# Kernel optimization log

Hardware: AMD Instinct MI355X
Metric: run time of the kernel (lower is better)

## Reference

```python
import jax, jax.numpy as jnp
import numpy as np

NUM_HEADS = 16

def setup_inputs() -> dict:
    key = jax.random.key(0)
    k1, k2, k3 = jax.random.split(key, 3)
    T, B, E = 2048, 4, 1024
    x = jax.random.normal(k1, (T, B, E), dtype=jnp.float32)
    # xavier-ish scale for weights
    in_proj_w = jax.random.normal(k2, (3 * E, E), dtype=jnp.float32) * (1.0 / np.sqrt(E))
    in_proj_b = jnp.zeros((3 * E,), dtype=jnp.float32)
    out_w = jax.random.normal(k3, (E, E), dtype=jnp.float32) * (1.0 / np.sqrt(E))
    out_b = jnp.zeros((E,), dtype=jnp.float32)
    return {"x": x, "in_proj_w": in_proj_w, "in_proj_b": in_proj_b, "out_w": out_w, "out_b": out_b}

def reference(x, in_proj_w, in_proj_b, out_w, out_b):
    # Self-attention (qkv_same path), dropout=0, eval mode, no masks.
    T, B, E = x.shape
    H = NUM_HEADS
    Dh = E // H
    scaling = Dh ** (-0.5)
    # fused in-projection: [T,B,3E]
    qkv = jnp.einsum('tbe,fe->tbf', x, in_proj_w) + in_proj_b
    q, k, v = jnp.split(qkv, 3, axis=-1)
    q = q * scaling
    # [T,B,E] -> [B,H,T,Dh]
    def to_heads(t):
        return t.reshape(T, B, H, Dh).transpose(1, 2, 0, 3)
    q, k, v = to_heads(q), to_heads(k), to_heads(v)
    # full TxT score matrix, softmax in float32 (matches F.softmax(..., dtype=float32))
    scores = jnp.einsum('bhtd,bhsd->bhts', q, k)
    attn_weights = jax.nn.softmax(scores.astype(jnp.float32), axis=-1).astype(scores.dtype)
    attn = jnp.einsum('bhts,bhsd->bhtd', attn_weights, v)
    # [B,H,T,Dh] -> [T,B,E]
    attn = attn.transpose(2, 0, 1, 3).reshape(T, B, E)
    attn = jnp.einsum('tbe,fe->tbf', attn, out_w) + out_b
    # need_weights=True: average over heads -> [B,T,T]
    avg_weights = attn_weights.sum(axis=1) / H
    return attn, avg_weights
```

## Files before the change

kernel.cpp:

```cpp
#include <hip/hip_runtime.h>
#include <stdint.h>

#define DEV __device__ __forceinline__

typedef __attribute__((ext_vector_type(8))) __bf16 bf16x8;
typedef __attribute__((ext_vector_type(4))) __bf16 bf16x4;
typedef __attribute__((ext_vector_type(4))) float f32x4;

DEV unsigned short f2bf(float f){
  union { float fv; unsigned u; } v; v.fv = f;
  unsigned r = v.u + 0x7fffu + ((v.u >> 16) & 1u);
  return (unsigned short)(r >> 16);
}

DEV void gload16(const void* g, void* l){
  __builtin_amdgcn_global_load_lds((const __attribute__((address_space(1))) void*)g,
                                   (__attribute__((address_space(3))) void*)l,
                                   16, 0, 0);
}

__global__ void k_cvt(const float* __restrict__ src, unsigned short* __restrict__ dst){
  const int i = (blockIdx.x * blockDim.x + threadIdx.x) << 2;
  const float4 v = *(const float4*)(src + i);
  ushort4 o;
  o.x = f2bf(v.x); o.y = f2bf(v.y); o.z = f2bf(v.z); o.w = f2bf(v.w);
  *(ushort4*)(dst + i) = o;
}

template<int MODE>
__launch_bounds__(256)
__global__ void k_gemm(const unsigned short* __restrict__ A,
                       const unsigned short* __restrict__ Bm,
                       const float* __restrict__ bias,
                       float* __restrict__ outF,
                       unsigned short* __restrict__ Qm,
                       unsigned short* __restrict__ Km,
                       unsigned short* __restrict__ VTm)
{
  __shared__ unsigned short As[128*64];
  __shared__ unsigned short Bs[128*64];
  const int tid  = threadIdx.x;
  const int lane = tid & 63;
  const int wid  = tid >> 6;
  const int wr   = wid >> 1;
  const int wc   = wid & 1;
  const int wg = blockIdx.x;
  int bx, by;
  if (MODE == 0){ const int slot = wg >> 3; bx = (wg & 7) + 8*(slot >> 6); by = slot & 63; }
  else          { bx = wg & 7; by = wg >> 3; }
  const int r0   = by * 128;
  const int c0   = bx * 128;
  const int l15  = lane & 15;
  const int l4   = lane >> 4;

  f32x4 acc[4][4];
#pragma unroll
  for (int m = 0; m < 4; ++m)
#pragma unroll
    for (int n = 0; n < 4; ++n)
      acc[m][n] = (f32x4){0.f, 0.f, 0.f, 0.f};

  for (int k0 = 0; k0 < 1024; k0 += 64){
#pragma unroll
    for (int i = 0; i < 4; ++i){
      const int sb   = (i*4 + wid)*64;
      const int slot = sb + lane;
      const int row  = slot >> 3;
      const int cg   = (slot & 7) ^ (row & 7);
      gload16(A  + (size_t)(r0 + row)*1024 + k0 + cg*8, (void*)(As + sb*8));
      gload16(Bm + (size_t)(c0 + row)*1024 + k0 + cg*8, (void*)(Bs + sb*8));
    }
    __syncthreads();
#pragma unroll
    for (int kk = 0; kk < 2; ++kk){
      bf16x8 af[4], bf[4];
#pragma unroll
      for (int m = 0; m < 4; ++m){
        const int row = wr*64 + m*16 + l15;
        const int ch  = (kk*4 + l4) ^ (row & 7);
        af[m] = *(const bf16x8*)(As + row*64 + ch*8);
      }
#pragma unroll
      for (int n = 0; n < 4; ++n){
        const int row = wc*64 + n*16 + l15;
        const int ch  = (kk*4 + l4) ^ (row & 7);
        bf[n] = *(const bf16x8*)(Bs + row*64 + ch*8);
      }
#pragma unroll
      for (int m = 0; m < 4; ++m)
#pragma unroll
        for (int n = 0; n < 4; ++n)
          acc[m][n] = __builtin_amdgcn_mfma_f32_16x16x32_bf16(af[m], bf[n], acc[m][n], 0, 0, 0);
    }
    __syncthreads();
  }

  if (MODE == 0){
#pragma unroll
    for (int n = 0; n < 4; ++n){
      const int f     = c0 + wc*64 + n*16 + l15;
      const float bs  = bias[f];
      const int which = f >> 10;
      const int fi    = f & 1023;
      const int h     = fi >> 6;
      const int d     = fi & 63;
#pragma unroll
      for (int m = 0; m < 4; ++m){
        const int rb = r0 + wr*64 + m*16 + (l4 << 2);
#pragma unroll
        for (int j = 0; j < 4; ++j){
          const int r = rb + j;
          const int t = r >> 2;
          const int b = r & 3;
          float v = acc[m][n][j] + bs;
          if (which == 0) v *= 0.18033688f;
          const unsigned short bv = f2bf(v);
          const int bh = b*16 + h;
          if (which == 0)      Qm [((size_t)bh*2048 + t)*64 + d] = bv;
          else if (which == 1) Km [((size_t)bh*2048 + t)*64 + d] = bv;
          else                 VTm[((size_t)bh*64 + d)*2048 + t] = bv;
        }
      }
    }
  } else {
#pragma unroll
    for (int m = 0; m < 4; ++m){
      const int rb = r0 + wr*64 + m*16 + (l4 << 2);
#pragma unroll
      for (int n = 0; n < 4; ++n){
        const int f    = c0 + wc*64 + n*16 + l15;
        const float bs = bias[f];
#pragma unroll
        for (int j = 0; j < 4; ++j)
          outF[(size_t)(rb + j)*1024 + f] = acc[m][n][j] + bs;
      }
    }
  }
}

__launch_bounds__(256)
__global__ void k_pv(const unsigned short* __restrict__ Qm,
                     const unsigned short* __restrict__ Km,
                     const unsigned short* __restrict__ VTm,
                     float* __restrict__ linv,
                     unsigned short* __restrict__ ctx)
{
  __shared__ unsigned short Ws[128*64];
  __shared__ unsigned short Ks[2][64*64];
  __shared__ unsigned short Vs[2][64*64];
  const int tid = threadIdx.x, lane = tid & 63, wid = tid >> 6;
  const int l15 = lane & 15, l4 = lane >> 4;
  const int wg = blockIdx.x;
  const int slotb = wg >> 3;
  const int bh = (wg & 7) + 8*(slotb >> 4);
  const int t0 = (slotb & 15) * 128;
  const unsigned short* Qb = Qm  + (size_t)bh*131072;
  const unsigned short* Kb = Km  + (size_t)bh*131072;
  const unsigned short* Vb = VTm + (size_t)bh*131072;

#pragma unroll
  for (int i = 0; i < 2; ++i){
    const int slot = i*256 + tid;
    const int row = slot >> 3;
    const int cg = (slot & 7) ^ (row & 7);
    gload16(Kb + (size_t)row*64 + cg*8, (void*)(Ks[0] + slot*8));
    gload16(Vb + (size_t)row*2048 + cg*8, (void*)(Vs[0] + slot*8));
  }
  bf16x8 aq[2][2];
#pragma unroll
  for (int qs = 0; qs < 2; ++qs)
#pragma unroll
    for (int kk = 0; kk < 2; ++kk)
      aq[qs][kk] = *(const bf16x8*)(Qb + (size_t)(t0 + wid*32 + qs*16 + l15)*64 + (kk*4 + l4)*8);
  __syncthreads();

  f32x4 oacc[2][4];
#pragma unroll
  for (int qs = 0; qs < 2; ++qs)
#pragma unroll
    for (int n = 0; n < 4; ++n) oacc[qs][n] = (f32x4){0.f,0.f,0.f,0.f};
  float lacc[2] = {0.f, 0.f};
  const int rx = l15 & 7;

  for (int s0 = 0; s0 < 2048; s0 += 64){
    const int cur = (s0 >> 6) & 1;
    if (s0 + 64 < 2048){
#pragma unroll
      for (int i = 0; i < 2; ++i){
        const int slot = i*256 + tid;
        const int row = slot >> 3;
        const int cg = (slot & 7) ^ (row & 7);
        gload16(Kb + (size_t)(s0 + 64 + row)*64 + cg*8, (void*)(Ks[cur^1] + slot*8));
        gload16(Vb + (size_t)row*2048 + (s0 + 64) + cg*8, (void*)(Vs[cur^1] + slot*8));
      }
    }
#pragma unroll
    for (int n = 0; n < 4; ++n){
      bf16x8 ak[2];
#pragma unroll
      for (int kk = 0; kk < 2; ++kk){
        const int ch = (kk*4 + l4) ^ rx;
        ak[kk] = *(const bf16x8*)(Ks[cur] + (n*16 + l15)*64 + ch*8);
      }
#pragma unroll
      for (int qs = 0; qs < 2; ++qs){
        f32x4 sacc = (f32x4){0.f,0.f,0.f,0.f};
        sacc = __builtin_amdgcn_mfma_f32_16x16x32_bf16(ak[0], aq[qs][0], sacc, 0, 0, 0);
        sacc = __builtin_amdgcn_mfma_f32_16x16x32_bf16(ak[1], aq[qs][1], sacc, 0, 0, 0);
        f32x4 pv;
        pv[0] = __builtin_amdgcn_exp2f(sacc[0]);
        pv[1] = __builtin_amdgcn_exp2f(sacc[1]);
        pv[2] = __builtin_amdgcn_exp2f(sacc[2]);
        pv[3] = __builtin_amdgcn_exp2f(sacc[3]);
        lacc[qs] += (pv[0] + pv[1]) + (pv[2] + pv[3]);
        const bf16x4 pb = __builtin_convertvector(pv, bf16x4);
        const int wrow = wid*32 + qs*16 + l15;
        const int g = (n*4 + l4) ^ (rx << 1);
        *(bf16x4*)(Ws + wrow*64 + g*4) = pb;
      }
    }
    bf16x8 aw[2][2];
#pragma unroll
    for (int qs = 0; qs < 2; ++qs)
#pragma unroll
      for (int kk = 0; kk < 2; ++kk){
        const int c = (kk*4 + l4) ^ rx;
        aw[qs][kk] = *(const bf16x8*)(Ws + (wid*32 + qs*16 + l15)*64 + c*8);
      }
#pragma unroll
    for (int n = 0; n < 4; ++n){
#pragma unroll
      for (int kk = 0; kk < 2; ++kk){
        const int ch = (kk*4 + l4) ^ rx;
        const bf16x8 bv = *(const bf16x8*)(Vs[cur] + (n*16 + l15)*64 + ch*8);
#pragma unroll
        for (int qs = 0; qs < 2; ++qs)
          oacc[qs][n] = __builtin_amdgcn_mfma_f32_16x16x32_bf16(aw[qs][kk], bv, oacc[qs][n], 0, 0, 0);
      }
    }
    __syncthreads();
  }

  const int b = bh >> 4, h = bh & 15;
#pragma unroll
  for (int qs = 0; qs < 2; ++qs){
    lacc[qs] += __shfl_xor(lacc[qs], 16);
    lacc[qs] += __shfl_xor(lacc[qs], 32);
    const float rl = 1.0f / lacc[qs];
    if (lane < 16)
      linv[(size_t)bh*2048 + t0 + wid*32 + qs*16 + lane] = rl;
    float rlj[4];
#pragma unroll
    for (int j = 0; j < 4; ++j)
      rlj[j] = __shfl(rl, (l4 << 2) + j);
#pragma unroll
    for (int n = 0; n < 4; ++n){
#pragma unroll
      for (int j = 0; j < 4; ++j){
        const int t = t0 + wid*32 + qs*16 + (l4 << 2) + j;
        const int d = n*16 + l15;
        ctx[((size_t)t*4 + b)*1024 + h*64 + d] = f2bf(oacc[qs][n][j] * rlj[j]);
      }
    }
  }
}

__launch_bounds__(256)
__global__ void k_avg(const unsigned short* __restrict__ Qm,
                      const unsigned short* __restrict__ Km,
                      const float* __restrict__ linv,
                      float* __restrict__ avg)
{
  __shared__ unsigned short Ks[2][128*64];
  const int tid = threadIdx.x, lane = tid & 63, wid = tid >> 6;
  const int l15 = lane & 15, l4 = lane >> 4;
  const int wg = blockIdx.x;
  const int slotb = wg >> 3;
  const int combo = (wg & 7) + 8*(slotb >> 5);
  const int b   = combo >> 4;
  const int s0  = (combo & 15) * 128;
  const int t0  = (slotb & 31) * 64;

  float wacc[8][4];
#pragma unroll
  for (int n = 0; n < 8; ++n)
#pragma unroll
    for (int j = 0; j < 4; ++j) wacc[n][j] = 0.f;

  {
    const unsigned short* Kb = Km + (size_t)(b*16)*131072;
#pragma unroll
    for (int i = 0; i < 4; ++i){
      const int slot = i*256 + tid;
      const int row = slot >> 3;
      const int cg = (slot & 7) ^ (row & 7);
      gload16(Kb + (size_t)(s0 + row)*64 + cg*8, (void*)(Ks[0] + slot*8));
    }
  }
  __syncthreads();

  for (int h = 0; h < 16; ++h){
    const int cur = h & 1;
    if (h < 15){
      const unsigned short* Kb = Km + (size_t)(b*16 + h + 1)*131072;
#pragma unroll
      for (int i = 0; i < 4; ++i){
        const int slot = i*256 + tid;
        const int row = slot >> 3;
        const int cg = (slot & 7) ^ (row & 7);
        gload16(Kb + (size_t)(s0 + row)*64 + cg*8, (void*)(Ks[cur^1] + slot*8));
      }
    }
    const int bh = b*16 + h;
    const unsigned short* Qb = Qm + (size_t)bh*131072;

    bf16x8 aq[2];
#pragma unroll
    for (int kk = 0; kk < 2; ++kk)
      aq[kk] = *(const bf16x8*)(Qb + (size_t)(t0 + wid*16 + l15)*64 + (kk*4 + l4)*8);

    float4 lj = *(const float4*)(linv + (size_t)bh*2048 + t0 + wid*16 + (l4 << 2));
    lj.x *= 0.0625f; lj.y *= 0.0625f; lj.z *= 0.0625f; lj.w *= 0.0625f;

#pragma unroll
    for (int n = 0; n < 8; ++n){
      f32x4 sacc = (f32x4){0.f,0.f,0.f,0.f};
#pragma unroll
      for (int kk = 0; kk < 2; ++kk){
        const int row = n*16 + l15;
        const int ch  = (kk*4 + l4) ^ (row & 7);
        const bf16x8 bk = *(const bf16x8*)(Ks[cur] + row*64 + ch*8);
        sacc = __builtin_amdgcn_mfma_f32_16x16x32_bf16(aq[kk], bk, sacc, 0, 0, 0);
      }
      wacc[n][0] += __builtin_amdgcn_exp2f(sacc[0]) * lj.x;
      wacc[n][1] += __builtin_amdgcn_exp2f(sacc[1]) * lj.y;
      wacc[n][2] += __builtin_amdgcn_exp2f(sacc[2]) * lj.z;
      wacc[n][3] += __builtin_amdgcn_exp2f(sacc[3]) * lj.w;
    }
    __syncthreads();
  }

#pragma unroll
  for (int n = 0; n < 8; ++n)
#pragma unroll
    for (int j = 0; j < 4; ++j){
      const int t = t0 + wid*16 + (l4 << 2) + j;
      const int s = s0 + n*16 + l15;
      avg[((size_t)b*2048 + t)*2048 + s] = wacc[n][j];
    }
}

extern "C" void kernel_launch(void* const* d_in, const int* in_sizes, int n_in,
                              void* d_out, int out_size, void* d_ws, size_t ws_size,
                              hipStream_t stream)
{
  const float* x    = (const float*)d_in[0];
  const float* wqkv = (const float*)d_in[1];
  const float* bqkv = (const float*)d_in[2];
  const float* wout = (const float*)d_in[3];
  const float* bout = (const float*)d_in[4];
  float* out = (float*)d_out;

  char* ws = (char*)d_ws;
  unsigned short* xb    = (unsigned short*)(ws);
  unsigned short* wqkvb = (unsigned short*)(ws + ((size_t)16 << 20));
  unsigned short* woutb = (unsigned short*)(ws + ((size_t)24 << 20));
  unsigned short* Qm    = (unsigned short*)(ws + ((size_t)26 << 20));
  unsigned short* Km    = (unsigned short*)(ws + ((size_t)42 << 20));
  unsigned short* VTm   = (unsigned short*)(ws + ((size_t)58 << 20));
  unsigned short* ctx   = (unsigned short*)(ws + ((size_t)74 << 20));
  float* linv = (float*)(ws + ((size_t)90 << 20));

  k_cvt<<<8192, 256, 0, stream>>>(x,    xb);
  k_cvt<<<3072, 256, 0, stream>>>(wqkv, wqkvb);
  k_cvt<<<1024, 256, 0, stream>>>(wout, woutb);

  k_gemm<0><<<1536, 256, 0, stream>>>(xb, wqkvb, bqkv, nullptr, Qm, Km, VTm);
  k_pv     <<<1024, 256, 0, stream>>>(Qm, Km, VTm, linv, ctx);
  k_avg    <<<2048, 256, 0, stream>>>(Qm, Km, linv, out + 8388608);
  k_gemm<1><<< 512, 256, 0, stream>>>(ctx, woutb, bout, out, nullptr, nullptr, nullptr);
}
```

Before: 306.3 us.

## Enlarge attention tiles: 512-thread PV blocks and two query subtiles in avg

k_pv now runs 512-thread blocks covering 256 query rows per (b,h), so each staged K/V tile in LDS is shared by twice as many waves and global K/V traffic is halved. k_avg has each wave handle two 16-row query subtiles against the same K tile, reusing K fragments across two MFMA chains and halving the grid. The cost is more registers per thread (doubled accumulators), fewer workgroups in flight, and a larger LDS footprint in k_pv.

```diff
diff --git a/kernel.cpp b/kernel.cpp
--- a/kernel.cpp
+++ b/kernel.cpp
@@ -138,33 +138,32 @@
   }
 }
 
-__launch_bounds__(256)
+__launch_bounds__(512)
 __global__ void k_pv(const unsigned short* __restrict__ Qm,
                      const unsigned short* __restrict__ Km,
                      const unsigned short* __restrict__ VTm,
                      float* __restrict__ linv,
                      unsigned short* __restrict__ ctx)
 {
-  __shared__ unsigned short Ws[128*64];
+  __shared__ unsigned short Ws[256*64];
   __shared__ unsigned short Ks[2][64*64];
   __shared__ unsigned short Vs[2][64*64];
   const int tid = threadIdx.x, lane = tid & 63, wid = tid >> 6;
   const int l15 = lane & 15, l4 = lane >> 4;
   const int wg = blockIdx.x;
-  const int slotb = wg >> 3;
-  const int bh = (wg & 7) + 8*(slotb >> 4);
-  const int t0 = (slotb & 15) * 128;
+  const int slot = wg >> 3;
+  const int bh = (wg & 7)*8 + (slot >> 3);
+  const int t0 = (slot & 7) * 256;
   const unsigned short* Qb = Qm  + (size_t)bh*131072;
   const unsigned short* Kb = Km  + (size_t)bh*131072;
   const unsigned short* Vb = VTm + (size_t)bh*131072;
 
-#pragma unroll
-  for (int i = 0; i < 2; ++i){
-    const int slot = i*256 + tid;
-    const int row = slot >> 3;
-    const int cg = (slot & 7) ^ (row & 7);
-    gload16(Kb + (size_t)row*64 + cg*8, (void*)(Ks[0] + slot*8));
-    gload16(Vb + (size_t)row*2048 + cg*8, (void*)(Vs[0] + slot*8));
+  {
+    const int s = tid;
+    const int row = s >> 3;
+    const int cg = (s & 7) ^ (row & 7);
+    gload16(Kb + (size_t)row*64 + cg*8, (void*)(Ks[0] + s*8));
+    gload16(Vb + (size_t)row*2048 + cg*8, (void*)(Vs[0] + s*8));
   }
   bf16x8 aq[2][2];
 #pragma unroll
@@ -185,14 +184,11 @@
   for (int s0 = 0; s0 < 2048; s0 += 64){
     const int cur = (s0 >> 6) & 1;
     if (s0 + 64 < 2048){
-#pragma unroll
-      for (int i = 0; i < 2; ++i){
-        const int slot = i*256 + tid;
-        const int row = slot >> 3;
-        const int cg = (slot & 7) ^ (row & 7);
-        gload16(Kb + (size_t)(s0 + 64 + row)*64 + cg*8, (void*)(Ks[cur^1] + slot*8));
-        gload16(Vb + (size_t)row*2048 + (s0 + 64) + cg*8, (void*)(Vs[cur^1] + slot*8));
-      }
+      const int s = tid;
+      const int row = s >> 3;
+      const int cg = (s & 7) ^ (row & 7);
+      gload16(Kb + (size_t)(s0 + 64 + row)*64 + cg*8, (void*)(Ks[cur^1] + s*8));
+      gload16(Vb + (size_t)row*2048 + (s0 + 64) + cg*8, (void*)(Vs[cur^1] + s*8));
     }
 #pragma unroll
     for (int n = 0; n < 4; ++n){
@@ -275,26 +271,29 @@
   const int tid = threadIdx.x, lane = tid & 63, wid = tid >> 6;
   const int l15 = lane & 15, l4 = lane >> 4;
   const int wg = blockIdx.x;
-  const int slotb = wg >> 3;
-  const int combo = (wg & 7) + 8*(slotb >> 5);
+  const int slot = wg >> 3;
+  const int combo = (wg & 7) + 8*(slot >> 4);
   const int b   = combo >> 4;
   const int s0  = (combo & 15) * 128;
-  const int t0  = (slotb & 31) * 64;
-
-  float wacc[8][4];
-#pragma unroll
-  for (int n = 0; n < 8; ++n)
-#pragma unroll
-    for (int j = 0; j < 4; ++j) wacc[n][j] = 0.f;
+  const int t0  = (slot & 15) * 128;
+  const int rx  = l15 & 7;
+
+  float wacc[2][8][4];
+#pragma unroll
+  for (int qs = 0; qs < 2; ++qs)
+#pragma unroll
+    for (int n = 0; n < 8; ++n)
+#pragma unroll
+      for (int j = 0; j < 4; ++j) wacc[qs][n][j] = 0.f;
 
   {
     const unsigned short* Kb = Km + (size_t)(b*16)*131072;
 #pragma unroll
     for (int i = 0; i < 4; ++i){
-      const int slot = i*256 + tid;
-      const int row = slot >> 3;
-      const int cg = (slot & 7) ^ (row & 7);
-      gload16(Kb + (size_t)(s0 + row)*64 + cg*8, (void*)(Ks[0] + slot*8));
+      const int s = i*256 + tid;
+      const int row = s >> 3;
+      const int cg = (s & 7) ^ (row & 7);
+      gload16(Kb + (size_t)(s0 + row)*64 + cg*8, (void*)(Ks[0] + s*8));
     }
   }
   __syncthreads();
@@ -305,49 +304,61 @@
       const unsigned short* Kb = Km + (size_t)(b*16 + h + 1)*131072;
 #pragma unroll
       for (int i = 0; i < 4; ++i){
-        const int slot = i*256 + tid;
-        const int row = slot >> 3;
-        const int cg = (slot & 7) ^ (row & 7);
-        gload16(Kb + (size_t)(s0 + row)*64 + cg*8, (void*)(Ks[cur^1] + slot*8));
+        const int s = i*256 + tid;
+        const int row = s >> 3;
+        const int cg = (s & 7) ^ (row & 7);
+        gload16(Kb + (size_t)(s0 + row)*64 + cg*8, (void*)(Ks[cur^1] + s*8));
       }
     }
     const int bh = b*16 + h;
     const unsigned short* Qb = Qm + (size_t)bh*131072;
 
-    bf16x8 aq[2];
-#pragma unroll
-    for (int kk = 0; kk < 2; ++kk)
-      aq[kk] = *(const bf16x8*)(Qb + (size_t)(t0 + wid*16 + l15)*64 + (kk*4 + l4)*8);
-
-    float4 lj = *(const float4*)(linv + (size_t)bh*2048 + t0 + wid*16 + (l4 << 2));
-    lj.x *= 0.0625f; lj.y *= 0.0625f; lj.z *= 0.0625f; lj.w *= 0.0625f;
+    bf16x8 aq[2][2];
+#pragma unroll
+    for (int qs = 0; qs < 2; ++qs)
+#pragma unroll
+      for (int kk = 0; kk < 2; ++kk)
+        aq[qs][kk] = *(const bf16x8*)(Qb + (size_t)(t0 + wid*32 + qs*16 + l15)*64 + (kk*4 + l4)*8);
+
+    float4 lj[2];
+#pragma unroll
+    for (int qs = 0; qs < 2; ++qs){
+      lj[qs] = *(const float4*)(linv + (size_t)bh*2048 + t0 + wid*32 + qs*16 + (l4 << 2));
+      lj[qs].x *= 0.0625f; lj[qs].y *= 0.0625f; lj[qs].z *= 0.0625f; lj[qs].w *= 0.0625f;
+    }
 
 #pragma unroll
     for (int n = 0; n < 8; ++n){
-      f32x4 sacc = (f32x4){0.f,0.f,0.f,0.f};
+      bf16x8 bk[2];
 #pragma unroll
       for (int kk = 0; kk < 2; ++kk){
-        const int row = n*16 + l15;
-        const int ch  = (kk*4 + l4) ^ (row & 7);
-        const bf16x8 bk = *(const bf16x8*)(Ks[cur] + row*64 + ch*8);
-        sacc = __builtin_amdgcn_mfma_f32_16x16x32_bf16(aq[kk], bk, sacc, 0, 0, 0);
-      }
-      wacc[n][0] += __builtin_amdgcn_exp2f(sacc[0]) * lj.x;
-      wacc[n][1] += __builtin_amdgcn_exp2f(sacc[1]) * lj.y;
-      wacc[n][2] += __builtin_amdgcn_exp2f(sacc[2]) * lj.z;
-      wacc[n][3] += __builtin_amdgcn_exp2f(sacc[3]) * lj.w;
+        const int ch = (kk*4 + l4) ^ rx;
+        bk[kk] = *(const bf16x8*)(Ks[cur] + (n*16 + l15)*64 + ch*8);
+      }
+#pragma unroll
+      for (int qs = 0; qs < 2; ++qs){
+        f32x4 sacc = (f32x4){0.f,0.f,0.f,0.f};
+        sacc = __builtin_amdgcn_mfma_f32_16x16x32_bf16(aq[qs][0], bk[0], sacc, 0, 0, 0);
+        sacc = __builtin_amdgcn_mfma_f32_16x16x32_bf16(aq[qs][1], bk[1], sacc, 0, 0, 0);
+        wacc[qs][n][0] += __builtin_amdgcn_exp2f(sacc[0]) * lj[qs].x;
+        wacc[qs][n][1] += __builtin_amdgcn_exp2f(sacc[1]) * lj[qs].y;
+        wacc[qs][n][2] += __builtin_amdgcn_exp2f(sacc[2]) * lj[qs].z;
+        wacc[qs][n][3] += __builtin_amdgcn_exp2f(sacc[3]) * lj[qs].w;
+      }
     }
     __syncthreads();
   }
 
 #pragma unroll
-  for (int n = 0; n < 8; ++n)
-#pragma unroll
-    for (int j = 0; j < 4; ++j){
-      const int t = t0 + wid*16 + (l4 << 2) + j;
-      const int s = s0 + n*16 + l15;
-      avg[((size_t)b*2048 + t)*2048 + s] = wacc[n][j];
-    }
+  for (int qs = 0; qs < 2; ++qs)
+#pragma unroll
+    for (int n = 0; n < 8; ++n)
+#pragma unroll
+      for (int j = 0; j < 4; ++j){
+        const int t = t0 + wid*32 + qs*16 + (l4 << 2) + j;
+        const int s = s0 + n*16 + l15;
+        avg[((size_t)b*2048 + t)*2048 + s] = wacc[qs][n][j];
+      }
 }
 
 extern "C" void kernel_launch(void* const* d_in, const int* in_sizes, int n_in,
@@ -376,7 +387,7 @@
   k_cvt<<<1024, 256, 0, stream>>>(wout, woutb);
 
   k_gemm<0><<<1536, 256, 0, stream>>>(xb, wqkvb, bqkv, nullptr, Qm, Km, VTm);
-  k_pv     <<<1024, 256, 0, stream>>>(Qm, Km, VTm, linv, ctx);
-  k_avg    <<<2048, 256, 0, stream>>>(Qm, Km, linv, out + 8388608);
+  k_pv     <<< 512, 512, 0, stream>>>(Qm, Km, VTm, linv, ctx);
+  k_avg    <<<1024, 256, 0, stream>>>(Qm, Km, linv, out + 8388608);
   k_gemm<1><<< 512, 256, 0, stream>>>(ctx, woutb, bout, out, nullptr, nullptr, nullptr);
 }
```

Measured after the change: 287.4 us. 6.2% less time.
